# Kernel optimization log

Hardware: AMD Instinct MI355X
Metric: run time of the kernel (lower is better)

The kernel has to match this reference:

```python
import jax, jax.numpy as jnp
import numpy as np

N_NODES = 100000
N_EDGES = 1200000
D_IN = 64
D_OUT = 64


def setup_inputs() -> dict:
    key = jax.random.key(0)
    ks = jax.random.split(key, 8)
    feat = jax.random.normal(ks[0], (N_NODES, D_IN), dtype=jnp.float32)
    src = jax.random.randint(ks[1], (N_EDGES,), 0, N_NODES, dtype=jnp.int32)
    dst = jax.random.randint(ks[2], (N_EDGES,), 0, N_NODES, dtype=jnp.int32)
    edge_weight = jax.random.uniform(ks[3], (N_EDGES, 1), dtype=jnp.float32)
    edge_mask = jax.random.uniform(ks[4], (N_EDGES, 1), dtype=jnp.float32)
    W_self = jax.random.normal(ks[5], (D_OUT, D_IN), dtype=jnp.float32) * (1.0 / np.sqrt(D_IN))
    b_self = jnp.zeros((D_OUT,), dtype=jnp.float32)
    W_neigh = jax.random.normal(ks[6], (D_OUT, D_IN), dtype=jnp.float32) * (1.0 / np.sqrt(D_IN))
    b_neigh = jnp.zeros((D_OUT,), dtype=jnp.float32)
    return {"feat": feat, "src": src, "dst": dst, "edge_weight": edge_weight,
            "edge_mask": edge_mask, "W_self": W_self, "b_self": b_self,
            "W_neigh": W_neigh, "b_neigh": b_neigh}


def reference(feat, src, dst, edge_weight, edge_mask, W_self, b_self, W_neigh, b_neigh):
    # message: gather src feats, scale by per-edge weight and mask  -> [E, D_IN]
    msg = feat[src] * edge_weight * edge_mask
    # mean scatter-reduce over incoming edges per dst node
    neigh_sum = jax.ops.segment_sum(msg, dst, num_segments=N_NODES)  # [N, D_IN]
    deg = jax.ops.segment_sum(jnp.ones((msg.shape[0],), dtype=feat.dtype), dst,
                              num_segments=N_NODES)  # [N]
    h_neigh = neigh_sum / jnp.maximum(deg, 1.0)[:, None]  # zero-degree nodes -> 0 (DGL mean semantics)
    # dual linear fuse
    rst = (feat @ W_self.T + b_self) + (h_neigh @ W_neigh.T + b_neigh)
    return rst
```

## Files before the change

### kernel.cpp

```cpp
#include <hip/hip_runtime.h>

#define NB_MAX   1568
#define CAP      1024
#define BT_EDGES 4096
#define BT_TPB   1024
#define EPE      4

typedef __attribute__((ext_vector_type(4))) float floatx4;
typedef __attribute__((ext_vector_type(2))) float floatx2;
typedef __attribute__((ext_vector_type(8))) short bf16x8;

__device__ __forceinline__ unsigned short f32_to_bf16(float f) {
  unsigned u = __float_as_uint(f);
  u = (u + 0x7fffu + ((u >> 16) & 1u)) >> 16;
  return (unsigned short)u;
}
__device__ __forceinline__ unsigned pack2(float a, float b) {
  return (unsigned)f32_to_bf16(a) | ((unsigned)f32_to_bf16(b) << 16);
}
__device__ __forceinline__ bf16x8 zero_bf16x8() {
  bf16x8 v;
#pragma unroll
  for (int i = 0; i < 8; ++i) v[i] = 0;
  return v;
}

#if __has_builtin(__builtin_amdgcn_cvt_pk_fp8_f32)
__device__ __forceinline__ unsigned pack_fp8x4(float a, float b, float c, float d) {
  unsigned v = (unsigned)__builtin_amdgcn_cvt_pk_fp8_f32(a, b, 0, false);
  v = (unsigned)__builtin_amdgcn_cvt_pk_fp8_f32(c, d, (int)v, true);
  return v;
}
#else
__device__ __forceinline__ unsigned sw_f32_fp8(float f) {
  unsigned u = __float_as_uint(f);
  unsigned s = (u >> 24) & 0x80u;
  unsigned au = u & 0x7fffffffu;
  if (au > 0x43E00000u) au = 0x43E00000u;
  au += 0x7FFFFu + ((au >> 20) & 1u);
  int e = (int)(au >> 23) - 120;
  if (e <= 0) return s;
  return s | ((unsigned)e << 3) | ((au >> 20) & 7u);
}
__device__ __forceinline__ unsigned pack_fp8x4(float a, float b, float c, float d) {
  return sw_f32_fp8(a) | (sw_f32_fp8(b) << 8) | (sw_f32_fp8(c) << 16) |
         (sw_f32_fp8(d) << 24);
}
#endif

#if __has_builtin(__builtin_amdgcn_cvt_pk_f32_fp8)
__device__ __forceinline__ void dec4(float* acc, unsigned w32, float wt) {
  floatx2 f0 = __builtin_amdgcn_cvt_pk_f32_fp8((int)w32, false);
  floatx2 f1 = __builtin_amdgcn_cvt_pk_f32_fp8((int)w32, true);
  acc[0] += wt * f0.x; acc[1] += wt * f0.y;
  acc[2] += wt * f1.x; acc[3] += wt * f1.y;
}
#else
__device__ __forceinline__ float sw_fp8_f32(unsigned b) {
  unsigned s = (b & 0x80u) << 24;
  unsigned e = (b >> 3) & 0xFu;
  unsigned m = b & 7u;
  float fn = __uint_as_float(s | ((e + 120u) << 23) | (m << 20));
  float fd = (float)(int)m * 0.001953125f;
  fd = (b & 0x80u) ? -fd : fd;
  return e ? fn : fd;
}
__device__ __forceinline__ void dec4(float* acc, unsigned w32, float wt) {
  acc[0] += wt * sw_fp8_f32(w32 & 0xFF);
  acc[1] += wt * sw_fp8_f32((w32 >> 8) & 0xFF);
  acc[2] += wt * sw_fp8_f32((w32 >> 16) & 0xFF);
  acc[3] += wt * sw_fp8_f32(w32 >> 24);
}
#endif

__global__ __launch_bounds__(BT_TPB) void k_build(
    const float* __restrict__ feat, const int* __restrict__ src,
    const int* __restrict__ dst, const float* __restrict__ ew,
    const float* __restrict__ em, const float* __restrict__ Ws,
    const float* __restrict__ Wn, int* __restrict__ gCursor,
    unsigned* __restrict__ recs, unsigned short* __restrict__ featb,
    unsigned char* __restrict__ featq, unsigned short* __restrict__ Wb,
    int E, int nChunks, int nB) {
  __shared__ unsigned stage[BT_EDGES];
  __shared__ unsigned short stageB[BT_EDGES];
  __shared__ int A[NB_MAX];
  __shared__ int B[NB_MAX];
  __shared__ int waveSums[16];

  const int t = threadIdx.x;
  const int lane = t & 63;
  const int wvid = t >> 6;
  const int e0 = blockIdx.x * BT_EDGES;
  const int eEnd = min(e0 + BT_EDGES, E);
  const int nLocal = eEnd - e0;

  for (int i = t; i < NB_MAX; i += BT_TPB) B[i] = 0;
  __syncthreads();

  int dreg[EPE];
#pragma unroll
  for (int k = 0; k < EPE; ++k) {
    int i = e0 + k * BT_TPB + t;
    dreg[k] = -1;
    if (i < eEnd) {
      int d = dst[i];
      dreg[k] = d;
      atomicAdd(&B[d >> 6], 1);
    }
  }
  __syncthreads();

  {
    const int EPT = 2;
    int b0 = t * EPT;
    int v[EPT];
    int sum = 0;
#pragma unroll
    for (int j = 0; j < EPT; ++j) {
      v[j] = (b0 + j < nB) ? B[b0 + j] : 0;
      sum += v[j];
    }
    int x = sum;
#pragma unroll
    for (int d = 1; d < 64; d <<= 1) {
      int y = __shfl_up(x, d, 64);
      if (lane >= d) x += y;
    }
    if (lane == 63) waveSums[wvid] = x;
    __syncthreads();
    int wprefix = 0;
    for (int i = 0; i < wvid; ++i) wprefix += waveSums[i];
    int run = wprefix + x - sum;
#pragma unroll
    for (int j = 0; j < EPT; ++j) {
      if (b0 + j < nB) A[b0 + j] = run;
      run += v[j];
    }
  }
  __syncthreads();

  for (int i = t; i < nB; i += BT_TPB) {
    int c = B[i];
    int l = A[i];
    int g = c ? atomicAdd(&gCursor[i], c) : 0;
    A[i] = i * CAP + g - l;
    B[i] = l;
  }
  __syncthreads();

#pragma unroll
  for (int k = 0; k < EPE; ++k) {
    int i = e0 + k * BT_TPB + t;
    if (i < eEnd) {
      int d = dreg[k];
      int bkt = d >> 6;
      int r = atomicAdd(&B[bkt], 1);
      float w = ew[i] * em[i];
      int wq = (int)(w * 511.0f + 0.5f);
      if (wq > 511) wq = 511;
      stage[r] = (unsigned)src[i] | ((unsigned)(d & 63) << 17) |
                 ((unsigned)wq << 23);
      stageB[r] = (unsigned short)bkt;
    }
  }
  __syncthreads();

  for (int i = t; i < nLocal; i += BT_TPB) {
    int bkt = stageB[i];
    int pos = A[bkt] + i;
    if (pos < (bkt + 1) * CAP)
      recs[pos] = stage[i];
  }

  for (int c = blockIdx.x * BT_TPB + t; c < nChunks; c += gridDim.x * BT_TPB) {
    const float4* fp = reinterpret_cast<const float4*>(feat) + (size_t)c * 2;
    float4 a = fp[0], b = fp[1];
    uint4 o;
    o.x = pack2(a.x, a.y);
    o.y = pack2(a.z, a.w);
    o.z = pack2(b.x, b.y);
    o.w = pack2(b.z, b.w);
    reinterpret_cast<uint4*>(featb)[c] = o;
    uint2 q8;
    q8.x = pack_fp8x4(a.x, a.y, a.z, a.w);
    q8.y = pack_fp8x4(b.x, b.y, b.z, b.w);
    reinterpret_cast<uint2*>(featq)[c] = q8;
  }

  if (blockIdx.x == 0) {
    for (int i = t; i < 1024; i += BT_TPB) {
      int j = i >> 4, c4 = i & 15;
      float4 w4 = reinterpret_cast<const float4*>(Ws)[i];
      float4 n4 = reinterpret_cast<const float4*>(Wn)[i];
      *reinterpret_cast<uint2*>(&Wb[j * 128 + c4 * 4]) =
          make_uint2(pack2(w4.x, w4.y), pack2(w4.z, w4.w));
      *reinterpret_cast<uint2*>(&Wb[j * 128 + 64 + c4 * 4]) =
          make_uint2(pack2(n4.x, n4.y), pack2(n4.z, n4.w));
    }
  }
}

__global__ __launch_bounds__(512) void sage_gather_gemm(
    const unsigned short* __restrict__ featb,
    const unsigned char* __restrict__ featq,
    const unsigned short* __restrict__ Wb, const int* __restrict__ gCursor,
    const unsigned* __restrict__ recs, const float* __restrict__ bs,
    const float* __restrict__ bn, float* __restrict__ out, int N) {
  __shared__ unsigned short An[64][72];
  __shared__ unsigned rawL[CAP];
  __shared__ unsigned srtL[CAP];
  __shared__ float pf[64][64];
  __shared__ int cntS[64], offS[64], curS[64];

  const int t = threadIdx.x;
  const int b = blockIdx.x;
  const int n0 = b * 64;
  const int base = b * CAP;
  const int cb = min(gCursor[b], CAP);

  for (int i = t; i < cb; i += 512) rawL[i] = recs[base + i];
  if (t < 64) cntS[t] = 0;
  __syncthreads();

  for (int i = t; i < cb; i += 512)
    atomicAdd(&cntS[(rawL[i] >> 17) & 63], 1);
  __syncthreads();

  if (t < 64) {
    int c = cntS[t];
    int x = c;
#pragma unroll
    for (int d = 1; d < 64; d <<= 1) {
      int y = __shfl_up(x, d, 64);
      if (t >= d) x += y;
    }
    offS[t] = x - c;
    curS[t] = x - c;
  }
  __syncthreads();

  for (int i = t; i < cb; i += 512) {
    unsigned r = rawL[i];
    int p = atomicAdd(&curS[(r >> 17) & 63], 1);
    srtL[p] = r;
  }
  __syncthreads();

  {
    const int nl = t >> 3;
    const int g  = (t >> 2) & 1;
    const int q  = t & 3;
    const int deg = cntS[nl], off = offS[nl];
    const int myN = (deg - g + 1) >> 1;
    float acc[16];
#pragma unroll
    for (int i = 0; i < 16; ++i) acc[i] = 0.f;
    const uint4* fq = reinterpret_cast<const uint4*>(featq);

    uint4 uC, uN;
    float wC = 0.f, wN = 0.f;
    if (myN > 0) {
      unsigned r0 = srtL[off + g];
      uC = fq[(size_t)(r0 & 0x1FFFF) * 4 + q];
      wC = (float)(r0 >> 23) * (1.0f / 511.0f);
    }
    if (myN > 1) {
      unsigned r1 = srtL[off + g + 2];
      uN = fq[(size_t)(r1 & 0x1FFFF) * 4 + q];
      wN = (float)(r1 >> 23) * (1.0f / 511.0f);
    }
    for (int m = 0; m < myN; ++m) {
      uint4 u = uC;
      float w = wC;
      uC = uN; wC = wN;
      if (m + 2 < myN) {
        unsigned rn = srtL[off + g + 2 * (m + 2)];
        uN = fq[(size_t)(rn & 0x1FFFF) * 4 + q];
        wN = (float)(rn >> 23) * (1.0f / 511.0f);
      }
      dec4(acc + 0, u.x, w);
      dec4(acc + 4, u.y, w);
      dec4(acc + 8, u.z, w);
      dec4(acc + 12, u.w, w);
    }

    if (g == 1) {
#pragma unroll
      for (int i = 0; i < 16; ++i) pf[nl][q * 16 + i] = acc[i];
    }
    __syncthreads();
    if (g == 0) {
      float inv = 1.0f / fmaxf((float)deg, 1.0f);
#pragma unroll
      for (int i = 0; i < 16; ++i) acc[i] = (acc[i] + pf[nl][q * 16 + i]) * inv;
      uint4 o0, o1;
      o0.x = pack2(acc[0], acc[1]);
      o0.y = pack2(acc[2], acc[3]);
      o0.z = pack2(acc[4], acc[5]);
      o0.w = pack2(acc[6], acc[7]);
      o1.x = pack2(acc[8], acc[9]);
      o1.y = pack2(acc[10], acc[11]);
      o1.z = pack2(acc[12], acc[13]);
      o1.w = pack2(acc[14], acc[15]);
      *reinterpret_cast<uint4*>(&An[nl][q * 16]) = o0;
      *reinterpret_cast<uint4*>(&An[nl][q * 16 + 8]) = o1;
    }
  }
  __syncthreads();

  const int wv8 = t >> 6;
  const int nt = wv8 & 3;
  const int jh = wv8 >> 2;
  const int ln = t & 63;
  const int col = ln & 15;
  const int quad = ln >> 4;
  const int gn = n0 + nt * 16 + col;

  floatx4 acc4[2];
#pragma unroll
  for (int jj = 0; jj < 2; ++jj) {
    int jt = jh * 2 + jj;
    float bb = bs[jt * 16 + col] + bn[jt * 16 + col];
    acc4[jj] = (floatx4){bb, bb, bb, bb};
  }

#pragma unroll
  for (int kk = 0; kk < 4; ++kk) {
    bf16x8 af;
    if (kk < 2) {
      if (gn < N) {
        af = *reinterpret_cast<const bf16x8*>(featb + (size_t)gn * 64 + kk * 32 + quad * 8);
      } else {
        af = zero_bf16x8();
      }
    } else {
      af = *reinterpret_cast<const bf16x8*>(&An[nt * 16 + col][(kk - 2) * 32 + quad * 8]);
    }
#pragma unroll
    for (int jj = 0; jj < 2; ++jj) {
      int jt = jh * 2 + jj;
      bf16x8 bf = *reinterpret_cast<const bf16x8*>(
          Wb + (jt * 16 + col) * 128 + kk * 32 + quad * 8);
      acc4[jj] = __builtin_amdgcn_mfma_f32_16x16x32_bf16(af, bf, acc4[jj], 0, 0, 0);
    }
  }

#pragma unroll
  for (int jj = 0; jj < 2; ++jj) {
    int jt = jh * 2 + jj;
#pragma unroll
    for (int r = 0; r < 4; ++r) {
      int m = quad * 4 + r;
      int g2 = n0 + nt * 16 + m;
      if (g2 < N) out[(size_t)g2 * 64 + jt * 16 + col] = acc4[jj][r];
    }
  }
}

extern "C" void kernel_launch(void* const* d_in, const int* in_sizes, int n_in,
                              void* d_out, int out_size, void* d_ws, size_t ws_size,
                              hipStream_t stream) {
  const float* feat = (const float*)d_in[0];
  const int*   src  = (const int*)d_in[1];
  const int*   dst  = (const int*)d_in[2];
  const float* ew   = (const float*)d_in[3];
  const float* em   = (const float*)d_in[4];
  const float* Ws   = (const float*)d_in[5];
  const float* bs   = (const float*)d_in[6];
  const float* Wn   = (const float*)d_in[7];
  const float* bn   = (const float*)d_in[8];
  float* out = (float*)d_out;

  const int N = in_sizes[0] / 64;
  const int E = in_sizes[1];
  const int nB = (N + 63) / 64;

  unsigned short* featb = (unsigned short*)d_ws;
  unsigned char*  featq = (unsigned char*)(featb + (size_t)N * 64);
  unsigned short* Wb    = (unsigned short*)(featq + (size_t)N * 64);
  unsigned* recs   = (unsigned*)(Wb + 64 * 128);
  int*      gCursor = (int*)(recs + (size_t)NB_MAX * CAP);

  hipMemsetAsync(gCursor, 0, NB_MAX * sizeof(int), stream);

  int nChunks = N * 8;
  int gB = (E + BT_EDGES - 1) / BT_EDGES;

  k_build<<<gB, BT_TPB, 0, stream>>>(feat, src, dst, ew, em, Ws, Wn,
                                     gCursor, recs, featb, featq, Wb,
                                     E, nChunks, nB);
  sage_gather_gemm<<<nB, 512, 0, stream>>>(featb, featq, Wb, gCursor, recs,
                                           bs, bn, out, N);
}
```

Before: 158.4 us.

## Sort nodes by degree for wave balance, vectorize fp8 accumulation, retune build chunk

The gather kernel ranks the 64 nodes in a block by in-degree and assigns them to 8-thread groups in sorted order. Each wavefront then handles nodes of similar degree, which reduces divergence from uneven neighbor loops. The per-edge accumulation now uses float2 vector math, which can map to packed FMA, and the partial-sum shared array is padded to reduce bank conflicts. The build kernel processes 5 edges per thread instead of 4, which raises its shared-memory staging footprint.

```diff
diff --git a/kernel.cpp b/kernel.cpp
--- a/kernel.cpp
+++ b/kernel.cpp
@@ -2,9 +2,9 @@
 
 #define NB_MAX   1568
 #define CAP      1024
-#define BT_EDGES 4096
+#define BT_EDGES 5120
 #define BT_TPB   1024
-#define EPE      4
+#define EPE      5
 
 typedef __attribute__((ext_vector_type(4))) float floatx4;
 typedef __attribute__((ext_vector_type(2))) float floatx2;
@@ -49,11 +49,11 @@
 #endif
 
 #if __has_builtin(__builtin_amdgcn_cvt_pk_f32_fp8)
-__device__ __forceinline__ void dec4(float* acc, unsigned w32, float wt) {
+__device__ __forceinline__ void dec4v(floatx2* acc, unsigned w32, floatx2 w2) {
   floatx2 f0 = __builtin_amdgcn_cvt_pk_f32_fp8((int)w32, false);
   floatx2 f1 = __builtin_amdgcn_cvt_pk_f32_fp8((int)w32, true);
-  acc[0] += wt * f0.x; acc[1] += wt * f0.y;
-  acc[2] += wt * f1.x; acc[3] += wt * f1.y;
+  acc[0] += w2 * f0;
+  acc[1] += w2 * f1;
 }
 #else
 __device__ __forceinline__ float sw_fp8_f32(unsigned b) {
@@ -65,11 +65,14 @@
   fd = (b & 0x80u) ? -fd : fd;
   return e ? fn : fd;
 }
-__device__ __forceinline__ void dec4(float* acc, unsigned w32, float wt) {
-  acc[0] += wt * sw_fp8_f32(w32 & 0xFF);
-  acc[1] += wt * sw_fp8_f32((w32 >> 8) & 0xFF);
-  acc[2] += wt * sw_fp8_f32((w32 >> 16) & 0xFF);
-  acc[3] += wt * sw_fp8_f32(w32 >> 24);
+__device__ __forceinline__ void dec4v(floatx2* acc, unsigned w32, floatx2 w2) {
+  floatx2 f0, f1;
+  f0.x = sw_fp8_f32(w32 & 0xFF);
+  f0.y = sw_fp8_f32((w32 >> 8) & 0xFF);
+  f1.x = sw_fp8_f32((w32 >> 16) & 0xFF);
+  f1.y = sw_fp8_f32(w32 >> 24);
+  acc[0] += w2 * f0;
+  acc[1] += w2 * f1;
 }
 #endif
 
@@ -209,8 +212,9 @@
   __shared__ unsigned short An[64][72];
   __shared__ unsigned rawL[CAP];
   __shared__ unsigned srtL[CAP];
-  __shared__ float pf[64][64];
+  __shared__ float pf[64][66];
   __shared__ int cntS[64], offS[64], curS[64];
+  __shared__ unsigned char permS[64];
 
   const int t = threadIdx.x;
   const int b = blockIdx.x;
@@ -236,6 +240,13 @@
     }
     offS[t] = x - c;
     curS[t] = x - c;
+    int rank = 0;
+#pragma unroll
+    for (int j = 0; j < 64; ++j) {
+      int dj = __shfl(c, j, 64);
+      rank += (int)((dj > c) | ((dj == c) & (j < t)));
+    }
+    permS[rank] = (unsigned char)t;
   }
   __syncthreads();
 
@@ -247,14 +258,15 @@
   __syncthreads();
 
   {
-    const int nl = t >> 3;
+    const int rl = t >> 3;
+    const int nl = permS[rl];
     const int g  = (t >> 2) & 1;
     const int q  = t & 3;
     const int deg = cntS[nl], off = offS[nl];
     const int myN = (deg - g + 1) >> 1;
-    float acc[16];
-#pragma unroll
-    for (int i = 0; i < 16; ++i) acc[i] = 0.f;
+    floatx2 acc2[8];
+#pragma unroll
+    for (int i = 0; i < 8; ++i) acc2[i] = (floatx2){0.f, 0.f};
     const uint4* fq = reinterpret_cast<const uint4*>(featq);
 
     uint4 uC, uN;
@@ -278,30 +290,34 @@
         uN = fq[(size_t)(rn & 0x1FFFF) * 4 + q];
         wN = (float)(rn >> 23) * (1.0f / 511.0f);
       }
-      dec4(acc + 0, u.x, w);
-      dec4(acc + 4, u.y, w);
-      dec4(acc + 8, u.z, w);
-      dec4(acc + 12, u.w, w);
+      floatx2 w2 = (floatx2){w, w};
+      dec4v(acc2 + 0, u.x, w2);
+      dec4v(acc2 + 2, u.y, w2);
+      dec4v(acc2 + 4, u.z, w2);
+      dec4v(acc2 + 6, u.w, w2);
     }
 
     if (g == 1) {
 #pragma unroll
-      for (int i = 0; i < 16; ++i) pf[nl][q * 16 + i] = acc[i];
+      for (int k = 0; k < 8; ++k)
+        *reinterpret_cast<floatx2*>(&pf[nl][q * 16 + 2 * k]) = acc2[k];
     }
     __syncthreads();
     if (g == 0) {
       float inv = 1.0f / fmaxf((float)deg, 1.0f);
-#pragma unroll
-      for (int i = 0; i < 16; ++i) acc[i] = (acc[i] + pf[nl][q * 16 + i]) * inv;
+      floatx2 inv2 = (floatx2){inv, inv};
+#pragma unroll
+      for (int k = 0; k < 8; ++k)
+        acc2[k] = (acc2[k] + *reinterpret_cast<floatx2*>(&pf[nl][q * 16 + 2 * k])) * inv2;
       uint4 o0, o1;
-      o0.x = pack2(acc[0], acc[1]);
-      o0.y = pack2(acc[2], acc[3]);
-      o0.z = pack2(acc[4], acc[5]);
-      o0.w = pack2(acc[6], acc[7]);
-      o1.x = pack2(acc[8], acc[9]);
-      o1.y = pack2(acc[10], acc[11]);
-      o1.z = pack2(acc[12], acc[13]);
-      o1.w = pack2(acc[14], acc[15]);
+      o0.x = pack2(acc2[0].x, acc2[0].y);
+      o0.y = pack2(acc2[1].x, acc2[1].y);
+      o0.z = pack2(acc2[2].x, acc2[2].y);
+      o0.w = pack2(acc2[3].x, acc2[3].y);
+      o1.x = pack2(acc2[4].x, acc2[4].y);
+      o1.y = pack2(acc2[5].x, acc2[5].y);
+      o1.z = pack2(acc2[6].x, acc2[6].y);
+      o1.w = pack2(acc2[7].x, acc2[7].y);
       *reinterpret_cast<uint4*>(&An[nl][q * 16]) = o0;
       *reinterpret_cast<uint4*>(&An[nl][q * 16 + 8]) = o1;
     }
```

After: 165.7 us. +4.7%, slower.

## Deepen gather prefetch to four edges and reduce halves via shuffle

Applied to the files above, without the earlier changes.

The per-node gather loop now keeps four outstanding feature loads per thread instead of two, using a 4-way unrolled loop where weights are zeroed to mask tail iterations. The two half-accumulators are combined with a cross-lane shuffle instead of a shared-memory buffer and an extra block barrier, which removes 16KB of LDS. The binning kernel also handles 5 edges per thread instead of 4. More registers are live, and tail iterations issue wasted FMA work.

```diff
diff --git a/kernel.cpp b/kernel.cpp
--- a/kernel.cpp
+++ b/kernel.cpp
@@ -2,9 +2,9 @@
 
 #define NB_MAX   1568
 #define CAP      1024
-#define BT_EDGES 4096
+#define BT_EDGES 5120
 #define BT_TPB   1024
-#define EPE      4
+#define EPE      5
 
 typedef __attribute__((ext_vector_type(4))) float floatx4;
 typedef __attribute__((ext_vector_type(2))) float floatx2;
@@ -209,7 +209,6 @@
   __shared__ unsigned short An[64][72];
   __shared__ unsigned rawL[CAP];
   __shared__ unsigned srtL[CAP];
-  __shared__ float pf[64][64];
   __shared__ int cntS[64], offS[64], curS[64];
 
   const int t = threadIdx.x;
@@ -252,47 +251,54 @@
     const int q  = t & 3;
     const int deg = cntS[nl], off = offS[nl];
     const int myN = (deg - g + 1) >> 1;
+    const int base2 = off + g;
     float acc[16];
 #pragma unroll
     for (int i = 0; i < 16; ++i) acc[i] = 0.f;
     const uint4* fq = reinterpret_cast<const uint4*>(featq);
 
-    uint4 uC, uN;
-    float wC = 0.f, wN = 0.f;
-    if (myN > 0) {
-      unsigned r0 = srtL[off + g];
-      uC = fq[(size_t)(r0 & 0x1FFFF) * 4 + q];
-      wC = (float)(r0 >> 23) * (1.0f / 511.0f);
-    }
-    if (myN > 1) {
-      unsigned r1 = srtL[off + g + 2];
-      uN = fq[(size_t)(r1 & 0x1FFFF) * 4 + q];
-      wN = (float)(r1 >> 23) * (1.0f / 511.0f);
-    }
-    for (int m = 0; m < myN; ++m) {
-      uint4 u = uC;
-      float w = wC;
-      uC = uN; wC = wN;
-      if (m + 2 < myN) {
-        unsigned rn = srtL[off + g + 2 * (m + 2)];
-        uN = fq[(size_t)(rn & 0x1FFFF) * 4 + q];
-        wN = (float)(rn >> 23) * (1.0f / 511.0f);
-      }
-      dec4(acc + 0, u.x, w);
-      dec4(acc + 4, u.y, w);
-      dec4(acc + 8, u.z, w);
-      dec4(acc + 12, u.w, w);
-    }
-
-    if (g == 1) {
-#pragma unroll
-      for (int i = 0; i < 16; ++i) pf[nl][q * 16 + i] = acc[i];
-    }
-    __syncthreads();
+    uint4 u0 = {0, 0, 0, 0}, u1 = {0, 0, 0, 0};
+    uint4 u2 = {0, 0, 0, 0}, u3 = {0, 0, 0, 0};
+    float w0 = 0.f, w1 = 0.f, w2 = 0.f, w3 = 0.f;
+
+#define PRELOAD(U, W, I)                                  \
+    if ((I) < myN) {                                      \
+      unsigned r_ = srtL[base2 + 2 * (I)];                \
+      U = fq[(size_t)(r_ & 0x1FFFF) * 4 + q];             \
+      W = (float)(r_ >> 23) * (1.0f / 511.0f);            \
+    }
+    PRELOAD(u0, w0, 0)
+    PRELOAD(u1, w1, 1)
+    PRELOAD(u2, w2, 2)
+    PRELOAD(u3, w3, 3)
+
+    for (int m = 0; m < myN; m += 4) {
+      dec4(acc + 0, u0.x, w0); dec4(acc + 4, u0.y, w0);
+      dec4(acc + 8, u0.z, w0); dec4(acc + 12, u0.w, w0);
+      w0 = 0.f;
+      PRELOAD(u0, w0, m + 4)
+      dec4(acc + 0, u1.x, w1); dec4(acc + 4, u1.y, w1);
+      dec4(acc + 8, u1.z, w1); dec4(acc + 12, u1.w, w1);
+      w1 = 0.f;
+      PRELOAD(u1, w1, m + 5)
+      dec4(acc + 0, u2.x, w2); dec4(acc + 4, u2.y, w2);
+      dec4(acc + 8, u2.z, w2); dec4(acc + 12, u2.w, w2);
+      w2 = 0.f;
+      PRELOAD(u2, w2, m + 6)
+      dec4(acc + 0, u3.x, w3); dec4(acc + 4, u3.y, w3);
+      dec4(acc + 8, u3.z, w3); dec4(acc + 12, u3.w, w3);
+      w3 = 0.f;
+      PRELOAD(u3, w3, m + 7)
+    }
+#undef PRELOAD
+
+#pragma unroll
+    for (int i = 0; i < 16; ++i) acc[i] += __shfl_xor(acc[i], 4, 64);
+
     if (g == 0) {
       float inv = 1.0f / fmaxf((float)deg, 1.0f);
 #pragma unroll
-      for (int i = 0; i < 16; ++i) acc[i] = (acc[i] + pf[nl][q * 16 + i]) * inv;
+      for (int i = 0; i < 16; ++i) acc[i] *= inv;
       uint4 o0, o1;
       o0.x = pack2(acc[0], acc[1]);
       o0.y = pack2(acc[2], acc[3]);
```

Result: no change. 160.0 us (+1.0%).
